# Kernel optimization log

Measured on AMD Instinct MI355X. Metric: run time of the kernel, lower is better.

Reference implementation:

```python
import jax, jax.numpy as jnp
import numpy as np

TEMPERATURE = 0.07
EPS = 1e-8  # torch cosine_similarity clamps the norm product at eps


def setup_inputs() -> dict:
    key = jax.random.key(0)
    k1, k2 = jax.random.split(key)
    B, D = 8192, 256
    u = jax.random.normal(k1, (B, D), dtype=jnp.float32)
    v = jax.random.normal(k2, (B, D), dtype=jnp.float32)
    return {"u": u, "v": v}


def _cos_sim_matrix(a, b):
    # pairwise cosine similarity: (a . b) / max(|a||b|, eps)
    dots = a @ b.T                                   # [B, B]
    an = jnp.linalg.norm(a, axis=-1)                 # [B]
    bn = jnp.linalg.norm(b, axis=-1)                 # [B]
    denom = jnp.maximum(an[:, None] * bn[None, :], EPS)
    return dots / denom


def reference(u, v):
    B = u.shape[0]
    sim_uv = _cos_sim_matrix(u, v) / TEMPERATURE     # [B, B]
    sim_uu = _cos_sim_matrix(u, u) / TEMPERATURE     # [B, B]
    eye = jnp.eye(B, dtype=bool)
    pos_loss = jnp.diagonal(sim_uv)                  # [B]
    neg_inf = jnp.array(-jnp.inf, dtype=sim_uv.dtype)
    # off-diagonal entries of both matrices, concatenated per row (2B-2 valid each)
    negative_sim = jnp.concatenate(
        [jnp.where(eye, neg_inf, sim_uv), jnp.where(eye, neg_inf, sim_uu)], axis=1
    )                                                # [B, 2B]
    neg_loss = jax.nn.logsumexp(negative_sim, axis=-1)  # [B]
    return (-pos_loss + neg_loss).mean()
```

## Files before the change

### kernel.cpp

```cpp
#include <hip/hip_runtime.h>
#include <hip/hip_bf16.h>
#include <stdint.h>

#define NB 8192
#define ND 256
#define NW 16384
#define BM 128
#define BN 64
#define NSTRIP 4
#define STRIPW 4096
#define NTILES (STRIPW / BN)
#define SQRT_INVT 3.7796447f

typedef __bf16 bf16x8 __attribute__((ext_vector_type(8)));
typedef float floatx4 __attribute__((ext_vector_type(4)));

__device__ __forceinline__ void gload_lds16(const void* g, void* l) {
    __builtin_amdgcn_global_load_lds(
        (const __attribute__((address_space(1))) unsigned int*)g,
        (__attribute__((address_space(3))) unsigned int*)l,
        16, 0, 0);
}

__global__ __launch_bounds__(512) void prep_kernel(
    const float* __restrict__ u, const float* __restrict__ v,
    __hip_bfloat16* __restrict__ W)
{
    const int t    = threadIdx.x;
    const int row  = blockIdx.x * 8 + (t >> 6);
    const int lane = t & 63;
    const float* src = (row < NB) ? (v + (size_t)row * ND)
                                  : (u + (size_t)(row - NB) * ND);
    float4 x = ((const float4*)src)[lane];
    float ss = x.x * x.x + x.y * x.y + x.z * x.z + x.w * x.w;
#pragma unroll
    for (int off = 1; off < 64; off <<= 1) ss += __shfl_xor(ss, off, 64);
    const float sc = rsqrtf(ss) * SQRT_INVT;
    ushort4 o;
    __hip_bfloat16 h;
    h = __float2bfloat16(x.x * sc); o.x = *(const unsigned short*)&h;
    h = __float2bfloat16(x.y * sc); o.y = *(const unsigned short*)&h;
    h = __float2bfloat16(x.z * sc); o.z = *(const unsigned short*)&h;
    h = __float2bfloat16(x.w * sc); o.w = *(const unsigned short*)&h;
    ((ushort4*)(W + (size_t)row * ND))[lane] = o;
}

__global__ __launch_bounds__(512, 2) void dcl_main(
    const __hip_bfloat16* __restrict__ W,
    float* __restrict__ partial,
    float* __restrict__ pos)
{
    const int b  = blockIdx.x;
    const int s  = (b >> 1) & 3;
    const int rt = ((b >> 3) << 1) | (b & 1);
    const int rb = rt * BM;

    const __hip_bfloat16* A = W + (size_t)NB * ND;

    __shared__ __align__(16) char lds[131072];

    const int tid  = threadIdx.x;
    const int wave = tid >> 6;
    const int lane = tid & 63;
    const int wm   = wave >> 2;
    const int wn   = wave & 3;
    const int quad = lane >> 4;
    const int tcol = lane & 15;
    const int cc   = lane & 31;
    const int rh   = lane >> 5;

#pragma unroll
    for (int i = 0; i < 8; i++) {
        int o = i * 8192 + wave * 1024 + lane * 16;
        int r = o >> 9;
        int c = (o >> 4) & 31;
        int cg = (c ^ (r & 15)) * 8;
        gload_lds16(A + (size_t)(rb + r) * ND + cg, lds + i * 8192 + wave * 1024);
    }
    __syncthreads();

    bf16x8 af[4][8];
#pragma unroll
    for (int mt = 0; mt < 4; mt++) {
        int r = wm * 64 + mt * 16 + tcol;
#pragma unroll
        for (int ks = 0; ks < 8; ks++) {
            int c = (ks * 4 + quad) ^ (r & 15);
            af[mt][ks] = *(const bf16x8*)(lds + r * 512 + (c << 4));
        }
    }
    __syncthreads();

    char* const wbuf  = lds + wave * 16384;
    const int   sbase = s * STRIPW;

    const bool isuv = (s < 2);
    int dp = rb + wm * 64 + (isuv ? 0 : NB);
    if ((dp >> 12) != s) dp = 0x40000000;

    float rsum[4][4];
#pragma unroll
    for (int mt = 0; mt < 4; mt++)
#pragma unroll
        for (int rg = 0; rg < 4; rg++) rsum[mt][rg] = 0.f;

#define STAGE(t, half) do {                                                  \
    const int rowb_ = sbase + (t) * BN + wn * 16;                            \
    char* dst_ = wbuf + (half) * 8192;                                       \
    _Pragma("unroll")                                                        \
    for (int i_ = 0; i_ < 8; i_++) {                                         \
        int r_ = 2 * i_ + rh;                                                \
        gload_lds16(W + (size_t)(rowb_ + r_) * ND + ((cc ^ r_) << 3),        \
                    dst_ + i_ * 1024);                                       \
    }                                                                        \
} while (0)

#define EPI_CLEAN(accP) do {                                                 \
    _Pragma("unroll")                                                        \
    for (int mt_ = 0; mt_ < 4; mt_++)                                        \
        _Pragma("unroll")                                                    \
        for (int rg_ = 0; rg_ < 4; rg_++)                                    \
            rsum[mt_][rg_] += __expf(accP[mt_][rg_]);                        \
} while (0)

#define FIXUP(accP, cbP) do {                                                \
    if ((cbP) == dp) {                                                       \
        _Pragma("unroll")                                                    \
        for (int mt_ = 0; mt_ < 4; mt_++)                                    \
            _Pragma("unroll")                                                \
            for (int rg_ = 0; rg_ < 4; rg_++) {                              \
                int rl_ = mt_ * 16 + quad * 4 + rg_;                         \
                bool sel_ = (rl_ == wn * 16 + tcol);                         \
                float sc_ = accP[mt_][rg_];                                  \
                if (isuv && sel_) pos[rb + wm * 64 + rl_] = sc_;             \
                if (sel_) rsum[mt_][rg_] -= __expf(sc_);                     \
            }                                                                \
    }                                                                        \
} while (0)

#define COMPUTE(acc, bufp) do {                                              \
    _Pragma("unroll")                                                        \
    for (int mt_ = 0; mt_ < 4; mt_++) acc[mt_] = (floatx4){0.f,0.f,0.f,0.f}; \
    __builtin_amdgcn_s_setprio(1);                                           \
    _Pragma("unroll")                                                        \
    for (int ks_ = 0; ks_ < 8; ks_++) {                                      \
        bf16x8 bb_ = *(const bf16x8*)((bufp) + tcol * 512 +                  \
                                      ((((ks_ * 4) + quad) ^ tcol) << 4));   \
        _Pragma("unroll")                                                    \
        for (int mt_ = 0; mt_ < 4; mt_++)                                    \
            acc[mt_] = __builtin_amdgcn_mfma_f32_16x16x32_bf16(              \
                af[mt_][ks_], bb_, acc[mt_], 0, 0, 0);                       \
    }                                                                        \
    __builtin_amdgcn_s_setprio(0);                                           \
} while (0)

    floatx4 accA[4], accB[4];
#pragma unroll
    for (int mt = 0; mt < 4; mt++)
        accB[mt] = (floatx4){-1e38f, -1e38f, -1e38f, -1e38f};
    int cbA = -1, cbB = -1;

    STAGE(0, 0);

#pragma unroll 1
    for (int t2 = 0; t2 < NTILES; t2 += 2) {
        asm volatile("s_waitcnt vmcnt(0)" ::: "memory");
        STAGE(t2 + 1, 1);
        __builtin_amdgcn_sched_barrier(0);
        EPI_CLEAN(accB);
        COMPUTE(accA, wbuf);
        __builtin_amdgcn_sched_barrier(0);
        FIXUP(accB, cbB);
        cbA = sbase + t2 * BN;

        asm volatile("s_waitcnt vmcnt(0)" ::: "memory");
        if (t2 + 2 < NTILES) STAGE(t2 + 2, 0);
        __builtin_amdgcn_sched_barrier(0);
        EPI_CLEAN(accA);
        COMPUTE(accB, wbuf + 8192);
        __builtin_amdgcn_sched_barrier(0);
        FIXUP(accA, cbA);
        cbB = sbase + (t2 + 1) * BN;
    }
    EPI_CLEAN(accB);
    FIXUP(accB, cbB);

#undef STAGE
#undef EPI_CLEAN
#undef FIXUP
#undef COMPUTE

    __syncthreads();

#pragma unroll
    for (int mt = 0; mt < 4; mt++)
#pragma unroll
        for (int reg = 0; reg < 4; reg++) {
            float vsum = rsum[mt][reg];
            vsum += __shfl_xor(vsum, 1, 64);
            vsum += __shfl_xor(vsum, 2, 64);
            vsum += __shfl_xor(vsum, 4, 64);
            vsum += __shfl_xor(vsum, 8, 64);
            if (tcol == 0) {
                int lrow = wm * 64 + mt * 16 + quad * 4 + reg;
                ((float*)lds)[wn * 128 + lrow] = vsum;
            }
        }
    __syncthreads();
    if (tid < BM) {
        const float* lf = (const float*)lds;
        float t = lf[tid] + lf[128 + tid] + lf[256 + tid] + lf[384 + tid];
        partial[(size_t)s * NB + rb + tid] = t;
    }
}

__global__ __launch_bounds__(1024) void finalize_kernel(
    const float* __restrict__ partial, const float* __restrict__ pos,
    float* __restrict__ out)
{
    const int t = threadIdx.x;
    float s = 0.f;
    for (int i = t; i < NB; i += 1024) {
        float tot = partial[i] + partial[NB + i] + partial[2 * NB + i]
                  + partial[3 * NB + i];
        s += logf(tot) - pos[i];
    }
#pragma unroll
    for (int off = 32; off > 0; off >>= 1) s += __shfl_down(s, off, 64);
    __shared__ float wsum[16];
    if ((t & 63) == 0) wsum[t >> 6] = s;
    __syncthreads();
    if (t == 0) {
        float tot = 0.f;
#pragma unroll
        for (int i = 0; i < 16; i++) tot += wsum[i];
        out[0] = tot / (float)NB;
    }
}

extern "C" void kernel_launch(void* const* d_in, const int* in_sizes, int n_in,
                              void* d_out, int out_size, void* d_ws, size_t ws_size,
                              hipStream_t stream) {
    const float* u = (const float*)d_in[0];
    const float* v = (const float*)d_in[1];
    float* out = (float*)d_out;

    char* ws = (char*)d_ws;
    __hip_bfloat16* W = (__hip_bfloat16*)ws;
    float* partial = (float*)(ws + (size_t)NW * ND * sizeof(__hip_bfloat16));
    float* pos     = partial + NSTRIP * NB;

    prep_kernel<<<NW / 8, 512, 0, stream>>>(u, v, W);
    dcl_main<<<256, 512, 0, stream>>>(W, partial, pos);
    finalize_kernel<<<1, 1024, 0, stream>>>(partial, pos, out);
}
```

Before: 137.4 us.

## Pipeline half-K B tiles through four-slot LDS ring with partial vmcnt waits

The main loop now stages each 64-column B tile as two half-K chunks into a 4-slot per-wave LDS ring, prefetching three chunks ahead and using partial vmcnt waits instead of draining all loads before each tile. The A fragments are loaded straight from global into registers, skipping the LDS round-trip and two block barriers. The diagonal is excluded in a single fused epilogue rather than by subtracting its exp afterwards. The finalize step is spread over 32 blocks that atomically add into an output zeroed by the prep kernel. This trades a simpler schedule for finer-grained load overlap, at the cost of more complex wait-count bookkeeping and a nondeterministic float atomic sum order.

```diff
diff --git a/kernel.cpp b/kernel.cpp
--- a/kernel.cpp
+++ b/kernel.cpp
@@ -10,6 +10,7 @@
 #define NSTRIP 4
 #define STRIPW 4096
 #define NTILES (STRIPW / BN)
+#define NU (NTILES * 2)
 #define SQRT_INVT 3.7796447f
 
 typedef __bf16 bf16x8 __attribute__((ext_vector_type(8)));
@@ -24,9 +25,10 @@
 
 __global__ __launch_bounds__(512) void prep_kernel(
     const float* __restrict__ u, const float* __restrict__ v,
-    __hip_bfloat16* __restrict__ W)
+    __hip_bfloat16* __restrict__ W, float* __restrict__ out)
 {
     const int t    = threadIdx.x;
+    if (blockIdx.x == 0 && t == 0) out[0] = 0.f;
     const int row  = blockIdx.x * 8 + (t >> 6);
     const int lane = t & 63;
     const float* src = (row < NB) ? (v + (size_t)row * ND)
@@ -66,129 +68,131 @@
     const int wn   = wave & 3;
     const int quad = lane >> 4;
     const int tcol = lane & 15;
-    const int cc   = lane & 31;
-    const int rh   = lane >> 5;
-
-#pragma unroll
-    for (int i = 0; i < 8; i++) {
-        int o = i * 8192 + wave * 1024 + lane * 16;
-        int r = o >> 9;
-        int c = (o >> 4) & 31;
-        int cg = (c ^ (r & 15)) * 8;
-        gload_lds16(A + (size_t)(rb + r) * ND + cg, lds + i * 8192 + wave * 1024);
-    }
-    __syncthreads();
-
-    bf16x8 af[4][8];
-#pragma unroll
-    for (int mt = 0; mt < 4; mt++) {
-        int r = wm * 64 + mt * 16 + tcol;
-#pragma unroll
-        for (int ks = 0; ks < 8; ks++) {
-            int c = (ks * 4 + quad) ^ (r & 15);
-            af[mt][ks] = *(const bf16x8*)(lds + r * 512 + (c << 4));
-        }
-    }
-    __syncthreads();
+    const int rh4  = lane >> 4;
+    const int cc   = lane & 15;
 
     char* const wbuf  = lds + wave * 16384;
     const int   sbase = s * STRIPW;
 
-    const bool isuv = (s < 2);
-    int dp = rb + wm * 64 + (isuv ? 0 : NB);
-    if ((dp >> 12) != s) dp = 0x40000000;
-
-    float rsum[4][4];
-#pragma unroll
-    for (int mt = 0; mt < 4; mt++)
-#pragma unroll
-        for (int rg = 0; rg < 4; rg++) rsum[mt][rg] = 0.f;
-
-#define STAGE(t, half) do {                                                  \
-    const int rowb_ = sbase + (t) * BN + wn * 16;                            \
-    char* dst_ = wbuf + (half) * 8192;                                       \
+#define STAGE(u) do {                                                        \
+    const int tu_ = (u) >> 1, h_ = (u) & 1;                                  \
+    const int rowb_ = sbase + tu_ * BN + wn * 16;                            \
+    char* dst_ = wbuf + ((u) & 3) * 4096;                                    \
     _Pragma("unroll")                                                        \
-    for (int i_ = 0; i_ < 8; i_++) {                                         \
-        int r_ = 2 * i_ + rh;                                                \
-        gload_lds16(W + (size_t)(rowb_ + r_) * ND + ((cc ^ r_) << 3),        \
+    for (int i_ = 0; i_ < 4; i_++) {                                         \
+        int r_ = i_ * 4 + rh4;                                               \
+        gload_lds16(W + (size_t)(rowb_ + r_) * ND + h_ * 128                 \
+                      + ((cc ^ r_) << 3),                                    \
                     dst_ + i_ * 1024);                                       \
     }                                                                        \
 } while (0)
 
-#define EPI_CLEAN(accP) do {                                                 \
+#define COMPUTE_HALF(u) do {                                                 \
+    const char* sb_ = wbuf + ((u) & 3) * 4096;                               \
+    const int h_ = (u) & 1;                                                  \
+    __builtin_amdgcn_s_setprio(1);                                           \
     _Pragma("unroll")                                                        \
-    for (int mt_ = 0; mt_ < 4; mt_++)                                        \
+    for (int ks_ = 0; ks_ < 4; ks_++) {                                      \
+        bf16x8 bb_ = *(const bf16x8*)(sb_ + tcol * 256 +                     \
+                                      ((((ks_ * 4) + quad) ^ tcol) << 4));   \
         _Pragma("unroll")                                                    \
-        for (int rg_ = 0; rg_ < 4; rg_++)                                    \
-            rsum[mt_][rg_] += __expf(accP[mt_][rg_]);                        \
-} while (0)
-
-#define FIXUP(accP, cbP) do {                                                \
-    if ((cbP) == dp) {                                                       \
+        for (int mt_ = 0; mt_ < 4; mt_++)                                    \
+            acc[mt_] = __builtin_amdgcn_mfma_f32_16x16x32_bf16(              \
+                af[mt_][h_ * 4 + ks_], bb_, acc[mt_], 0, 0, 0);              \
+    }                                                                        \
+    __builtin_amdgcn_s_setprio(0);                                           \
+} while (0)
+
+#define ACC_INIT() do {                                                      \
+    _Pragma("unroll")                                                        \
+    for (int mt_ = 0; mt_ < 4; mt_++) acc[mt_] = (floatx4){0.f,0.f,0.f,0.f}; \
+} while (0)
+
+#define WAITV(n) do {                                                        \
+    asm volatile("s_waitcnt vmcnt(" #n ")" ::: "memory");                    \
+    __builtin_amdgcn_sched_barrier(0);                                       \
+} while (0)
+
+#define EPILOGUE(t) do {                                                     \
+    const int cb_ = sbase + (t) * BN;                                        \
+    if (cb_ != dp) {                                                         \
+        _Pragma("unroll")                                                    \
+        for (int mt_ = 0; mt_ < 4; mt_++)                                    \
+            _Pragma("unroll")                                                \
+            for (int rg_ = 0; rg_ < 4; rg_++)                                \
+                rsum[mt_][rg_] += __expf(acc[mt_][rg_]);                     \
+    } else {                                                                 \
         _Pragma("unroll")                                                    \
         for (int mt_ = 0; mt_ < 4; mt_++)                                    \
             _Pragma("unroll")                                                \
             for (int rg_ = 0; rg_ < 4; rg_++) {                              \
                 int rl_ = mt_ * 16 + quad * 4 + rg_;                         \
                 bool sel_ = (rl_ == wn * 16 + tcol);                         \
-                float sc_ = accP[mt_][rg_];                                  \
+                float sc_ = acc[mt_][rg_];                                   \
                 if (isuv && sel_) pos[rb + wm * 64 + rl_] = sc_;             \
-                if (sel_) rsum[mt_][rg_] -= __expf(sc_);                     \
+                rsum[mt_][rg_] += sel_ ? 0.f : __expf(sc_);                  \
             }                                                                \
     }                                                                        \
 } while (0)
 
-#define COMPUTE(acc, bufp) do {                                              \
-    _Pragma("unroll")                                                        \
-    for (int mt_ = 0; mt_ < 4; mt_++) acc[mt_] = (floatx4){0.f,0.f,0.f,0.f}; \
-    __builtin_amdgcn_s_setprio(1);                                           \
-    _Pragma("unroll")                                                        \
-    for (int ks_ = 0; ks_ < 8; ks_++) {                                      \
-        bf16x8 bb_ = *(const bf16x8*)((bufp) + tcol * 512 +                  \
-                                      ((((ks_ * 4) + quad) ^ tcol) << 4));   \
-        _Pragma("unroll")                                                    \
-        for (int mt_ = 0; mt_ < 4; mt_++)                                    \
-            acc[mt_] = __builtin_amdgcn_mfma_f32_16x16x32_bf16(              \
-                af[mt_][ks_], bb_, acc[mt_], 0, 0, 0);                       \
-    }                                                                        \
-    __builtin_amdgcn_s_setprio(0);                                           \
-} while (0)
-
-    floatx4 accA[4], accB[4];
+    STAGE(0); STAGE(1); STAGE(2);
+
+    bf16x8 af[4][8];
+#pragma unroll
+    for (int mt = 0; mt < 4; mt++) {
+        const __hip_bfloat16* ar =
+            A + (size_t)(rb + wm * 64 + mt * 16 + tcol) * ND + quad * 8;
+#pragma unroll
+        for (int ks = 0; ks < 8; ks++)
+            af[mt][ks] = *(const bf16x8*)(ar + ks * 32);
+    }
+
+    const bool isuv = (s < 2);
+    int dp = rb + wm * 64 + (isuv ? 0 : NB);
+    if ((dp >> 12) != s) dp = 0x40000000;
+
+    float rsum[4][4];
 #pragma unroll
     for (int mt = 0; mt < 4; mt++)
-        accB[mt] = (floatx4){-1e38f, -1e38f, -1e38f, -1e38f};
-    int cbA = -1, cbB = -1;
-
-    STAGE(0, 0);
+#pragma unroll
+        for (int rg = 0; rg < 4; rg++) rsum[mt][rg] = 0.f;
+
+    floatx4 acc[4];
 
 #pragma unroll 1
-    for (int t2 = 0; t2 < NTILES; t2 += 2) {
-        asm volatile("s_waitcnt vmcnt(0)" ::: "memory");
-        STAGE(t2 + 1, 1);
+    for (int t = 0; t < NTILES - 2; t++) {
+        const int u0 = 2 * t;
+        ACC_INIT();
+        STAGE(u0 + 3);
+        WAITV(12);
+        COMPUTE_HALF(u0);
+        STAGE(u0 + 4);
+        WAITV(12);
+        COMPUTE_HALF(u0 + 1);
         __builtin_amdgcn_sched_barrier(0);
-        EPI_CLEAN(accB);
-        COMPUTE(accA, wbuf);
+        EPILOGUE(t);
+    }
+    {
+        ACC_INIT();
+        STAGE(127);
+        WAITV(12); COMPUTE_HALF(124);
+        WAITV(8);  COMPUTE_HALF(125);
         __builtin_amdgcn_sched_barrier(0);
-        FIXUP(accB, cbB);
-        cbA = sbase + t2 * BN;
-
-        asm volatile("s_waitcnt vmcnt(0)" ::: "memory");
-        if (t2 + 2 < NTILES) STAGE(t2 + 2, 0);
+        EPILOGUE(62);
+    }
+    {
+        ACC_INIT();
+        WAITV(4);  COMPUTE_HALF(126);
+        WAITV(0);  COMPUTE_HALF(127);
         __builtin_amdgcn_sched_barrier(0);
-        EPI_CLEAN(accA);
-        COMPUTE(accB, wbuf + 8192);
-        __builtin_amdgcn_sched_barrier(0);
-        FIXUP(accA, cbA);
-        cbB = sbase + (t2 + 1) * BN;
-    }
-    EPI_CLEAN(accB);
-    FIXUP(accB, cbB);
+        EPILOGUE(63);
+    }
 
 #undef STAGE
-#undef EPI_CLEAN
-#undef FIXUP
-#undef COMPUTE
+#undef COMPUTE_HALF
+#undef ACC_INIT
+#undef WAITV
+#undef EPILOGUE
 
     __syncthreads();
 
@@ -214,27 +218,23 @@
     }
 }
 
-__global__ __launch_bounds__(1024) void finalize_kernel(
+__global__ __launch_bounds__(256) void finalize_kernel(
     const float* __restrict__ partial, const float* __restrict__ pos,
     float* __restrict__ out)
 {
+    const int i = blockIdx.x * 256 + threadIdx.x;
+    float tot = partial[i] + partial[NB + i] + partial[2 * NB + i]
+              + partial[3 * NB + i];
+    float sv = logf(tot) - pos[i];
+#pragma unroll
+    for (int off = 32; off > 0; off >>= 1) sv += __shfl_down(sv, off, 64);
+    __shared__ float wsum[4];
     const int t = threadIdx.x;
-    float s = 0.f;
-    for (int i = t; i < NB; i += 1024) {
-        float tot = partial[i] + partial[NB + i] + partial[2 * NB + i]
-                  + partial[3 * NB + i];
-        s += logf(tot) - pos[i];
-    }
-#pragma unroll
-    for (int off = 32; off > 0; off >>= 1) s += __shfl_down(s, off, 64);
-    __shared__ float wsum[16];
-    if ((t & 63) == 0) wsum[t >> 6] = s;
+    if ((t & 63) == 0) wsum[t >> 6] = sv;
     __syncthreads();
     if (t == 0) {
-        float tot = 0.f;
-#pragma unroll
-        for (int i = 0; i < 16; i++) tot += wsum[i];
-        out[0] = tot / (float)NB;
+        float blk = (wsum[0] + wsum[1]) + (wsum[2] + wsum[3]);
+        atomicAdd(out, blk / (float)NB);
     }
 }
 
@@ -250,7 +250,7 @@
     float* partial = (float*)(ws + (size_t)NW * ND * sizeof(__hip_bfloat16));
     float* pos     = partial + NSTRIP * NB;
 
-    prep_kernel<<<NW / 8, 512, 0, stream>>>(u, v, W);
+    prep_kernel<<<NW / 8, 512, 0, stream>>>(u, v, W, out);
     dcl_main<<<256, 512, 0, stream>>>(W, partial, pos);
-    finalize_kernel<<<1, 1024, 0, stream>>>(partial, pos, out);
-}
+    finalize_kernel<<<NB / 256, 256, 0, stream>>>(partial, pos, out);
+}
```

After: 144.7 us. +5.3%, slower.
